# Kernel tuning notes

Hardware: AMD Instinct MI355X
Metric: run time of the kernel (lower is better)

## Reference

```python
import jax, jax.numpy as jnp
import numpy as np

LARGE_NEG = -1000000000.0
D_MODEL = 1024
NUM_HEADS = 16
DEPTH = D_MODEL // NUM_HEADS


def setup_inputs() -> dict:
    key = jax.random.key(0)
    ks = jax.random.split(key, 12)
    B, S, D = 4, 2048, D_MODEL
    scale = 1.0 / np.sqrt(D)
    inp = {
        "v": jax.random.normal(ks[0], (B, S, D), jnp.float32),
        "k": jax.random.normal(ks[1], (B, S, D), jnp.float32),
        "q": jax.random.normal(ks[2], (B, S, D), jnp.float32),
        "mask": jax.random.randint(ks[3], (B, 1, 1, S), 0, 2, jnp.int32),
        "Wq": jax.random.normal(ks[4], (D, D), jnp.float32) * scale,
        "bq": jnp.zeros((D,), jnp.float32),
        "Wk": jax.random.normal(ks[5], (D, D), jnp.float32) * scale,
        "bk": jnp.zeros((D,), jnp.float32),
        "Wv": jax.random.normal(ks[6], (D, D), jnp.float32) * scale,
        "bv": jnp.zeros((D,), jnp.float32),
        "Wo": jax.random.normal(ks[7], (D, D), jnp.float32) * scale,
        "bo": jnp.zeros((D,), jnp.float32),
    }
    return inp


def _split_heads(x):
    # [B, S, D] -> [B, H, S, depth]
    B, S, _ = x.shape
    return x.reshape(B, S, NUM_HEADS, DEPTH).transpose(0, 2, 1, 3)


def reference(v, k, q, mask, Wq, bq, Wk, bk, Wv, bv, Wo, bo):
    B, Sq, D = q.shape
    qh = _split_heads(q @ Wq + bq)  # [B,H,Sq,d]
    kh = _split_heads(k @ Wk + bk)  # [B,H,Sk,d]
    vh = _split_heads(v @ Wv + bv)  # [B,H,Sk,d]
    logits = jnp.einsum('bhqd,bhkd->bhqk', qh, kh) / jnp.sqrt(
        jnp.asarray(DEPTH, jnp.float32))
    logits = logits + mask.astype(jnp.float32) * LARGE_NEG
    attn = jax.nn.softmax(logits, axis=-1)
    ctx = jnp.einsum('bhqk,bhkd->bhqd', attn, vh)
    ctx = ctx.transpose(0, 2, 1, 3).reshape(B, Sq, D)  # concat heads
    return ctx @ Wo + bo
```

## Files before the change

kernel.cpp:

```cpp
#include <hip/hip_runtime.h>


typedef unsigned short ushort_t;
typedef __bf16          b16x8 __attribute__((ext_vector_type(8)));
typedef unsigned short  u16x8 __attribute__((ext_vector_type(8)));
typedef unsigned short  u16x4 __attribute__((ext_vector_type(4)));
typedef unsigned int    u32x4 __attribute__((ext_vector_type(4)));
typedef float           f32x4 __attribute__((ext_vector_type(4)));

#define B_ 4
#define S_ 2048
#define D_ 1024
#define H_ 16
#define DEPTH_ 64
#define LOG2E 1.4426950408889634f

__device__ __forceinline__ unsigned short f2bf(float f) {
  unsigned u = __builtin_bit_cast(unsigned, f);
  u += 0x7FFFu + ((u >> 16) & 1u);
  return (unsigned short)(u >> 16);
}

__device__ __forceinline__ unsigned pack_trunc(float lo, float hi) {
#if __has_builtin(__builtin_amdgcn_perm)
  return __builtin_amdgcn_perm(__builtin_bit_cast(unsigned, hi),
                               __builtin_bit_cast(unsigned, lo), 0x07060302u);
#else
  return (__builtin_bit_cast(unsigned, hi) & 0xFFFF0000u) |
         (__builtin_bit_cast(unsigned, lo) >> 16);
#endif
}

#if __has_builtin(__builtin_amdgcn_exp2f)
#define EXP2F(x) __builtin_amdgcn_exp2f(x)
#else
#define EXP2F(x) exp2f(x)
#endif

#define GLD16(gp, lp) __builtin_amdgcn_global_load_lds( \
    (__attribute__((address_space(1))) void*)(gp),       \
    (__attribute__((address_space(3))) void*)(lp), 16, 0, 0)

#define MFMA_BF16(a, b, c) __builtin_amdgcn_mfma_f32_16x16x32_bf16( \
    __builtin_bit_cast(b16x8, (a)), __builtin_bit_cast(b16x8, (b)), (c), 0, 0, 0)


__global__ void cvt_acts_kernel(const float* __restrict__ q, const float* __restrict__ k,
                                const float* __restrict__ v,
                                ushort_t* __restrict__ qb, ushort_t* __restrict__ kb,
                                ushort_t* __restrict__ vb) {
  const float* src = blockIdx.y == 0 ? q : blockIdx.y == 1 ? k : v;
  ushort_t*    dst = blockIdx.y == 0 ? qb : blockIdx.y == 1 ? kb : vb;
  size_t i = ((size_t)blockIdx.x * 256 + threadIdx.x) * 4;
  float4 f = *(const float4*)(src + i);
  u16x4 o;
  o[0] = f2bf(f.x); o[1] = f2bf(f.y); o[2] = f2bf(f.z); o[3] = f2bf(f.w);
  *(u16x4*)(dst + i) = o;
}

__global__ void cvt_wt_kernel(const float* __restrict__ Wq, const float* __restrict__ Wk,
                              const float* __restrict__ Wv, const float* __restrict__ Wo,
                              ushort_t* __restrict__ Wqt, ushort_t* __restrict__ Wkt,
                              ushort_t* __restrict__ Wvt, ushort_t* __restrict__ Wot) {
  __shared__ float t[32][33];
  const int z = blockIdx.y;
  const float* W = z == 0 ? Wq : z == 1 ? Wk : z == 2 ? Wv : Wo;
  ushort_t*   Wt = z == 0 ? Wqt : z == 1 ? Wkt : z == 2 ? Wvt : Wot;
  const int x = threadIdx.x & 31, y0 = threadIdx.x >> 5;
  const int kt = (blockIdx.x & 31) * 32, nt = (blockIdx.x >> 5) * 32;
#pragma unroll
  for (int r = 0; r < 4; r++) {
    int row = y0 + r * 8;
    t[row][x] = W[(size_t)(kt + row) * D_ + nt + x];
  }
  __syncthreads();
#pragma unroll
  for (int r = 0; r < 4; r++) {
    int row = y0 + r * 8;
    Wt[(size_t)(nt + row) * D_ + kt + x] = f2bf(t[x][row]);
  }
}


__device__ __forceinline__ void gemm_core(const ushort_t* __restrict__ A,
                                          const ushort_t* __restrict__ Bt,
                                          ushort_t* As, ushort_t* Bs,
                                          int tm, int tn, f32x4* acc) {
  const int tid = threadIdx.x;
  const int lane = tid & 63, wid = tid >> 6;
  const int wm = (wid >> 1) * 64, wn = (wid & 1) * 64;
  const int srow = lane >> 2;
  const int scolL = ((lane & 3) ^ ((srow >> 1) & 3)) * 8;
  const int c0 = wid * 2, c1 = c0 + 1;
  const ushort_t* ga0 = A  + (size_t)(tm + c0 * 16 + srow) * D_ + scolL;
  const ushort_t* ga1 = A  + (size_t)(tm + c1 * 16 + srow) * D_ + scolL;
  const ushort_t* gb0 = Bt + (size_t)(tn + c0 * 16 + srow) * D_ + scolL;
  const ushort_t* gb1 = Bt + (size_t)(tn + c1 * 16 + srow) * D_ + scolL;
  ushort_t* lA0 = As + c0 * 512; ushort_t* lA1 = As + c1 * 512;
  ushort_t* lB0 = Bs + c0 * 512; ushort_t* lB1 = Bs + c1 * 512;
  const int fr = lane & 15;
  const int fswz = ((lane >> 4) ^ ((fr >> 1) & 3)) * 8;
#pragma unroll
  for (int i = 0; i < 16; i++) acc[i] = f32x4{0.f, 0.f, 0.f, 0.f};
  for (int k0 = 0; k0 < D_; k0 += 32) {
    __syncthreads();
    GLD16(ga0 + k0, lA0);
    GLD16(ga1 + k0, lA1);
    GLD16(gb0 + k0, lB0);
    GLD16(gb1 + k0, lB1);
    __syncthreads();
    u16x8 af[4], bf[4];
#pragma unroll
    for (int mi = 0; mi < 4; mi++) af[mi] = *(const u16x8*)(As + (wm + mi * 16 + fr) * 32 + fswz);
#pragma unroll
    for (int ni = 0; ni < 4; ni++) bf[ni] = *(const u16x8*)(Bs + (wn + ni * 16 + fr) * 32 + fswz);
#pragma unroll
    for (int mi = 0; mi < 4; mi++)
#pragma unroll
      for (int ni = 0; ni < 4; ni++)
        acc[mi * 4 + ni] = MFMA_BF16(af[mi], bf[ni], acc[mi * 4 + ni]);
  }
}

__device__ __forceinline__ int sigma32(int k5) {
  return ((k5 & 15) >> 2) * 8 + ((k5 >> 4) & 1) * 4 + (k5 & 3);
}

__global__ __launch_bounds__(256, 2) void qkv_gemm_kernel(
    const ushort_t* __restrict__ qb, const ushort_t* __restrict__ kb, const ushort_t* __restrict__ vb,
    const ushort_t* __restrict__ Wqt, const ushort_t* __restrict__ Wkt, const ushort_t* __restrict__ Wvt,
    const float* __restrict__ bq, const float* __restrict__ bk, const float* __restrict__ bv,
    ushort_t* __restrict__ Qh, ushort_t* __restrict__ Kh, ushort_t* __restrict__ Vht) {
  __shared__ __align__(16) ushort_t smem[128 * 136];
  ushort_t* As = smem;
  ushort_t* Bs = smem + 4096;
  const int z = blockIdx.z;
  const ushort_t* A  = z == 0 ? qb : z == 1 ? kb : vb;
  const ushort_t* Bt = z == 0 ? Wqt : z == 1 ? Wkt : Wvt;
  const float* bias  = z == 0 ? bq : z == 1 ? bk : bv;
  const int tn = blockIdx.x * 128, tm = blockIdx.y * 128;
  f32x4 acc[16];
  gemm_core(A, Bt, As, Bs, tm, tn, acc);
  const int lane = threadIdx.x & 63, wid = threadIdx.x >> 6;
  const int wm = (wid >> 1) * 64, wn = (wid & 1) * 64;
  const int fr = lane & 15, rq = (lane >> 4) * 4;
  if (z == 2) {
    __syncthreads();
    ushort_t* trans = smem;
#pragma unroll
    for (int ni = 0; ni < 4; ni++) {
      const int n = wn + ni * 16 + fr;
      const float bb = bias[tn + n];
#pragma unroll
      for (int mi = 0; mi < 4; mi++) {
#pragma unroll
        for (int r = 0; r < 4; r++) {
          const int m = wm + mi * 16 + rq + r;
          const int mp = (m & ~31) + sigma32(m & 31);
          trans[n * 136 + mp] = f2bf(acc[mi * 4 + ni][r] + bb);
        }
      }
    }
    __syncthreads();
    const int n = threadIdx.x >> 1, hf = threadIdx.x & 1;
    const int col = tn + n, hh = col >> 6, dd = col & 63;
    const int bI = tm >> 11, sb = (tm & 2047) + hf * 64;
    ushort_t* dst = Vht + ((size_t)(bI * H_ + hh) * DEPTH_ + dd) * S_ + sb;
    const ushort_t* srcp = trans + n * 136 + hf * 64;
#pragma unroll
    for (int i = 0; i < 8; i++)
      *(u16x8*)(dst + i * 8) = *(const u16x8*)(srcp + i * 8);
  } else {
    ushort_t* outp = (z == 0) ? Qh : Kh;
    const float qscale = (z == 0) ? 0.125f * LOG2E : 1.0f;
#pragma unroll
    for (int ni = 0; ni < 4; ni++) {
      const int col = tn + wn + ni * 16 + fr;
      const float bb = bias[col];
      const int h = col >> 6, dd = col & 63;
#pragma unroll
      for (int mi = 0; mi < 4; mi++) {
#pragma unroll
        for (int r = 0; r < 4; r++) {
          const int m = tm + wm + mi * 16 + rq + r;
          const int b = m >> 11, s = m & 2047;
          outp[((size_t)(b * H_ + h) * S_ + s) * DEPTH_ + dd] =
              f2bf((acc[mi * 4 + ni][r] + bb) * qscale);
        }
      }
    }
  }
}

__global__ __launch_bounds__(256, 2) void out_gemm_kernel(
    const ushort_t* __restrict__ ctx, const ushort_t* __restrict__ Wot,
    const float* __restrict__ bo, float* __restrict__ out) {
  __shared__ __align__(16) ushort_t As[4096], Bs[4096];
  const int tn = blockIdx.x * 128, tm = blockIdx.y * 128;
  f32x4 acc[16];
  gemm_core(ctx, Wot, As, Bs, tm, tn, acc);
  const int lane = threadIdx.x & 63, wid = threadIdx.x >> 6;
  const int wm = (wid >> 1) * 64, wn = (wid & 1) * 64;
  const int fr = lane & 15, rq = (lane >> 4) * 4;
#pragma unroll
  for (int ni = 0; ni < 4; ni++) {
    const int col = tn + wn + ni * 16 + fr;
    const float bb = bo[col];
#pragma unroll
    for (int mi = 0; mi < 4; mi++) {
#pragma unroll
      for (int r = 0; r < 4; r++) {
        const int m = tm + wm + mi * 16 + rq + r;
        out[(size_t)m * D_ + col] = acc[mi * 4 + ni][r] + bb;
      }
    }
  }
}


__global__ __launch_bounds__(256, 4) void attn_kernel(
    const ushort_t* __restrict__ Qh, const ushort_t* __restrict__ Kh,
    const ushort_t* __restrict__ Vht, const int* __restrict__ mask,
    ushort_t* __restrict__ ctx) {
  __shared__ __align__(16) ushort_t Ks[128 * 64];
  __shared__ __align__(16) ushort_t Vs[64 * 128];
  __shared__ __align__(16) float Cm[2048];
  const int tid = threadIdx.x, lane = tid & 63, wid = tid >> 6;
  const int qt = blockIdx.x, bh = blockIdx.y;
  const int b = bh >> 4, h = bh & 15;
  const size_t base = (size_t)bh * (S_ * DEPTH_);
  const int fr = lane & 15, fq = lane >> 4;

  const int* mrow = mask + b * S_;
#pragma unroll
  for (int i = 0; i < 8; i++) {
    const int idx = tid + i * 256;
    Cm[idx] = mrow[idx] ? -1.4427e9f : 0.0f;
  }

  u16x8 qf[2][2];
#pragma unroll
  for (int nq = 0; nq < 2; nq++)
#pragma unroll
    for (int kc = 0; kc < 2; kc++)
      qf[nq][kc] = *(const u16x8*)(Qh + base +
          (size_t)(qt * 128 + wid * 32 + nq * 16 + fr) * DEPTH_ + kc * 32 + fq * 8);

  u16x8 ones_f;
  {
    const unsigned short o = (fr == 0) ? (unsigned short)0x3F80 : (unsigned short)0;
#pragma unroll
    for (int j = 0; j < 8; j++) ones_f[j] = o;
  }

  f32x4 Oa[4][2];
  f32x4 lacc[2];
#pragma unroll
  for (int di = 0; di < 4; di++)
#pragma unroll
    for (int nq = 0; nq < 2; nq++) Oa[di][nq] = f32x4{0.f, 0.f, 0.f, 0.f};
#pragma unroll
  for (int nq = 0; nq < 2; nq++) lacc[nq] = f32x4{0.f, 0.f, 0.f, 0.f};

  const int krow = lane >> 3;
  const int kcolL = ((lane & 7) ^ (krow & 7)) * 8;
  const int vrowc = lane >> 4;
  const int koff0 = ((0 + fq) ^ (fr & 7)) * 8;
  const int koff1 = ((4 + fq) ^ (fr & 7)) * 8;

  for (int kt = 0; kt < 16; kt++) {
    __syncthreads();
#pragma unroll
    for (int c = 0; c < 4; c++) {
      const int ch = wid * 4 + c;
      GLD16(Kh + base + (size_t)(kt * 128 + ch * 8 + krow) * DEPTH_ + kcolL, Ks + ch * 512);
      const int vrow = ch * 4 + vrowc;
      const int vcolL = ((lane & 15) ^ (vrow & 15)) * 8;
      GLD16(Vht + base + (size_t)vrow * S_ + kt * 128 + vcolL, Vs + ch * 512);
    }
    __syncthreads();

#pragma unroll
    for (int ks = 0; ks < 4; ks++) {
      const int nk0 = ks * 2, nk1 = nk0 + 1;
      const ushort_t* kr0 = Ks + (nk0 * 16 + fr) * 64;
      const ushort_t* kr1 = Ks + (nk1 * 16 + fr) * 64;
      const u16x8 a00 = *(const u16x8*)(kr0 + koff0);
      const u16x8 a01 = *(const u16x8*)(kr0 + koff1);
      const u16x8 a10 = *(const u16x8*)(kr1 + koff0);
      const u16x8 a11 = *(const u16x8*)(kr1 + koff1);
      f32x4 st0[2], st1[2];
#pragma unroll
      for (int nq = 0; nq < 2; nq++) {
        f32x4 t = f32x4{0.f, 0.f, 0.f, 0.f};
        t = MFMA_BF16(a00, qf[nq][0], t);
        t = MFMA_BF16(a01, qf[nq][1], t);
        st0[nq] = t;
        f32x4 u = f32x4{0.f, 0.f, 0.f, 0.f};
        u = MFMA_BF16(a10, qf[nq][0], u);
        u = MFMA_BF16(a11, qf[nq][1], u);
        st1[nq] = u;
      }
      const f32x4 cm0 = *(const f32x4*)(Cm + kt * 128 + nk0 * 16 + fq * 4);
      const f32x4 cm1 = *(const f32x4*)(Cm + kt * 128 + nk1 * 16 + fq * 4);
      u16x8 pb[2];
#pragma unroll
      for (int nq = 0; nq < 2; nq++) {
#pragma unroll
        for (int r = 0; r < 4; r++) {
          st0[nq][r] = EXP2F(st0[nq][r] + cm0[r]);
          st1[nq][r] = EXP2F(st1[nq][r] + cm1[r]);
        }
        u32x4 pk;
        pk[0] = pack_trunc(st0[nq][0], st0[nq][1]);
        pk[1] = pack_trunc(st0[nq][2], st0[nq][3]);
        pk[2] = pack_trunc(st1[nq][0], st1[nq][1]);
        pk[3] = pack_trunc(st1[nq][2], st1[nq][3]);
        pb[nq] = __builtin_bit_cast(u16x8, pk);
      }
      const int voff = ((ks * 4 + fq) ^ fr) * 8;
#pragma unroll
      for (int di = 0; di < 4; di++) {
        const u16x8 vf = *(const u16x8*)(Vs + (di * 16 + fr) * 128 + voff);
#pragma unroll
        for (int nq = 0; nq < 2; nq++)
          Oa[di][nq] = MFMA_BF16(vf, pb[nq], Oa[di][nq]);
      }
#pragma unroll
      for (int nq = 0; nq < 2; nq++)
        lacc[nq] = MFMA_BF16(ones_f, pb[nq], lacc[nq]);
    }
  }

#pragma unroll
  for (int nq = 0; nq < 2; nq++) {
    const int lv = __builtin_amdgcn_ds_bpermute(fr * 4, __builtin_bit_cast(int, lacc[nq][0]));
    const float inv = 1.0f / __builtin_bit_cast(float, lv);
    const int sg = qt * 128 + wid * 32 + nq * 16 + fr;
    ushort_t* crow = ctx + ((size_t)(b * S_ + sg)) * D_ + h * DEPTH_;
#pragma unroll
    for (int di = 0; di < 4; di++) {
      u16x4 o4;
#pragma unroll
      for (int r = 0; r < 4; r++) o4[r] = f2bf(Oa[di][nq][r] * inv);
      *(u16x4*)(crow + di * 16 + fq * 4) = o4;
    }
  }
}


extern "C" void kernel_launch(void* const* d_in, const int* in_sizes, int n_in,
                              void* d_out, int out_size, void* d_ws, size_t ws_size,
                              hipStream_t stream) {
  const float* v  = (const float*)d_in[0];
  const float* k  = (const float*)d_in[1];
  const float* q  = (const float*)d_in[2];
  const int* mask = (const int*)d_in[3];
  const float* Wq = (const float*)d_in[4];
  const float* bq = (const float*)d_in[5];
  const float* Wk = (const float*)d_in[6];
  const float* bk = (const float*)d_in[7];
  const float* Wv = (const float*)d_in[8];
  const float* bv = (const float*)d_in[9];
  const float* Wo = (const float*)d_in[10];
  const float* bo = (const float*)d_in[11];
  float* out = (float*)d_out;

  char* ws = (char*)d_ws;
  ushort_t* qb  = (ushort_t*)(ws);
  ushort_t* kb  = (ushort_t*)(ws + (size_t)(16u << 20));
  ushort_t* vb  = (ushort_t*)(ws + (size_t)(32u << 20));
  ushort_t* Wqt = (ushort_t*)(ws + (size_t)(48u << 20));
  ushort_t* Wkt = (ushort_t*)(ws + (size_t)(50u << 20));
  ushort_t* Wvt = (ushort_t*)(ws + (size_t)(52u << 20));
  ushort_t* Wot = (ushort_t*)(ws + (size_t)(54u << 20));
  ushort_t* Qh  = (ushort_t*)(ws + (size_t)(56u << 20));
  ushort_t* Kh  = (ushort_t*)(ws + (size_t)(72u << 20));
  ushort_t* Vht = (ushort_t*)(ws + (size_t)(88u << 20));
  ushort_t* ctx = qb;

  cvt_acts_kernel<<<dim3(8192, 3), 256, 0, stream>>>(q, k, v, qb, kb, vb);
  cvt_wt_kernel<<<dim3(1024, 4), 256, 0, stream>>>(Wq, Wk, Wv, Wo, Wqt, Wkt, Wvt, Wot);
  qkv_gemm_kernel<<<dim3(8, 64, 3), 256, 0, stream>>>(qb, kb, vb, Wqt, Wkt, Wvt,
                                                      bq, bk, bv, Qh, Kh, Vht);
  attn_kernel<<<dim3(16, 64), 256, 0, stream>>>(Qh, Kh, Vht, mask, ctx);
  out_gemm_kernel<<<dim3(8, 64), 256, 0, stream>>>(ctx, Wot, bo, out);
}
```

Measured before the change: 354.3 us.

## Double GEMM K-step to 64 and remap blocks across XCDs for cache locality

The shared GEMM core now loads a 64-wide K slice per iteration with an XOR-swizzled 64-column layout, which halves the number of barrier pairs per tile. The QKV and output GEMMs, and the attention kernel, switch to 1D grids whose block index is remapped so that blocks landing on the same XCD share the same A rows or the same batch-head. This aims to improve L2 reuse on the chiplet layout. The GEMMs also request occupancy 3 and use twice as much LDS per block, which may limit how many blocks actually fit per CU and adds register pressure.

```diff
diff --git a/kernel.cpp b/kernel.cpp
--- a/kernel.cpp
+++ b/kernel.cpp
@@ -89,36 +89,44 @@
   const int tid = threadIdx.x;
   const int lane = tid & 63, wid = tid >> 6;
   const int wm = (wid >> 1) * 64, wn = (wid & 1) * 64;
-  const int srow = lane >> 2;
-  const int scolL = ((lane & 3) ^ ((srow >> 1) & 3)) * 8;
-  const int c0 = wid * 2, c1 = c0 + 1;
-  const ushort_t* ga0 = A  + (size_t)(tm + c0 * 16 + srow) * D_ + scolL;
-  const ushort_t* ga1 = A  + (size_t)(tm + c1 * 16 + srow) * D_ + scolL;
-  const ushort_t* gb0 = Bt + (size_t)(tn + c0 * 16 + srow) * D_ + scolL;
-  const ushort_t* gb1 = Bt + (size_t)(tn + c1 * 16 + srow) * D_ + scolL;
-  ushort_t* lA0 = As + c0 * 512; ushort_t* lA1 = As + c1 * 512;
-  ushort_t* lB0 = Bs + c0 * 512; ushort_t* lB1 = Bs + c1 * 512;
-  const int fr = lane & 15;
-  const int fswz = ((lane >> 4) ^ ((fr >> 1) & 3)) * 8;
+  const int srow = lane >> 3;
+  const int scol = ((lane & 7) ^ srow) * 8;
+  const ushort_t* gA[4];
+  const ushort_t* gB[4];
+#pragma unroll
+  for (int c = 0; c < 4; c++) {
+    const int ch = wid * 4 + c;
+    gA[c] = A  + (size_t)(tm + ch * 8 + srow) * D_ + scol;
+    gB[c] = Bt + (size_t)(tn + ch * 8 + srow) * D_ + scol;
+  }
+  const int fr = lane & 15, fq = lane >> 4;
 #pragma unroll
   for (int i = 0; i < 16; i++) acc[i] = f32x4{0.f, 0.f, 0.f, 0.f};
-  for (int k0 = 0; k0 < D_; k0 += 32) {
-    __syncthreads();
-    GLD16(ga0 + k0, lA0);
-    GLD16(ga1 + k0, lA1);
-    GLD16(gb0 + k0, lB0);
-    GLD16(gb1 + k0, lB1);
-    __syncthreads();
-    u16x8 af[4], bf[4];
-#pragma unroll
-    for (int mi = 0; mi < 4; mi++) af[mi] = *(const u16x8*)(As + (wm + mi * 16 + fr) * 32 + fswz);
-#pragma unroll
-    for (int ni = 0; ni < 4; ni++) bf[ni] = *(const u16x8*)(Bs + (wn + ni * 16 + fr) * 32 + fswz);
-#pragma unroll
-    for (int mi = 0; mi < 4; mi++)
+  for (int k0 = 0; k0 < D_; k0 += 64) {
+    __syncthreads();
+#pragma unroll
+    for (int c = 0; c < 4; c++) {
+      const int ch = wid * 4 + c;
+      GLD16(gA[c] + k0, As + ch * 512);
+      GLD16(gB[c] + k0, Bs + ch * 512);
+    }
+    __syncthreads();
+#pragma unroll
+    for (int kh = 0; kh < 2; kh++) {
+      const int coff = (((kh * 4 + fq) ^ (fr & 7))) * 8;
+      u16x8 af[4], bf[4];
+#pragma unroll
+      for (int mi = 0; mi < 4; mi++)
+        af[mi] = *(const u16x8*)(As + (wm + mi * 16 + fr) * 64 + coff);
 #pragma unroll
       for (int ni = 0; ni < 4; ni++)
-        acc[mi * 4 + ni] = MFMA_BF16(af[mi], bf[ni], acc[mi * 4 + ni]);
+        bf[ni] = *(const u16x8*)(Bs + (wn + ni * 16 + fr) * 64 + coff);
+#pragma unroll
+      for (int mi = 0; mi < 4; mi++)
+#pragma unroll
+        for (int ni = 0; ni < 4; ni++)
+          acc[mi * 4 + ni] = MFMA_BF16(af[mi], bf[ni], acc[mi * 4 + ni]);
+    }
   }
 }
 
@@ -126,19 +134,26 @@
   return ((k5 & 15) >> 2) * 8 + ((k5 >> 4) & 1) * 4 + (k5 & 3);
 }
 
-__global__ __launch_bounds__(256, 2) void qkv_gemm_kernel(
+__device__ __forceinline__ void gemm_tile_swizzle(int bx, int& tm, int& tn) {
+  const int xcd = bx & 7, j = bx >> 3;
+  tn = (j & 7) * 128;
+  tm = (((j >> 3) << 3) | xcd) * 128;
+}
+
+__global__ __launch_bounds__(256, 3) void qkv_gemm_kernel(
     const ushort_t* __restrict__ qb, const ushort_t* __restrict__ kb, const ushort_t* __restrict__ vb,
     const ushort_t* __restrict__ Wqt, const ushort_t* __restrict__ Wkt, const ushort_t* __restrict__ Wvt,
     const float* __restrict__ bq, const float* __restrict__ bk, const float* __restrict__ bv,
     ushort_t* __restrict__ Qh, ushort_t* __restrict__ Kh, ushort_t* __restrict__ Vht) {
   __shared__ __align__(16) ushort_t smem[128 * 136];
   ushort_t* As = smem;
-  ushort_t* Bs = smem + 4096;
+  ushort_t* Bs = smem + 8192;
   const int z = blockIdx.z;
   const ushort_t* A  = z == 0 ? qb : z == 1 ? kb : vb;
   const ushort_t* Bt = z == 0 ? Wqt : z == 1 ? Wkt : Wvt;
   const float* bias  = z == 0 ? bq : z == 1 ? bk : bv;
-  const int tn = blockIdx.x * 128, tm = blockIdx.y * 128;
+  int tm, tn;
+  gemm_tile_swizzle(blockIdx.x, tm, tn);
   f32x4 acc[16];
   gemm_core(A, Bt, As, Bs, tm, tn, acc);
   const int lane = threadIdx.x & 63, wid = threadIdx.x >> 6;
@@ -192,11 +207,12 @@
   }
 }
 
-__global__ __launch_bounds__(256, 2) void out_gemm_kernel(
+__global__ __launch_bounds__(256, 3) void out_gemm_kernel(
     const ushort_t* __restrict__ ctx, const ushort_t* __restrict__ Wot,
     const float* __restrict__ bo, float* __restrict__ out) {
-  __shared__ __align__(16) ushort_t As[4096], Bs[4096];
-  const int tn = blockIdx.x * 128, tm = blockIdx.y * 128;
+  __shared__ __align__(16) ushort_t As[8192], Bs[8192];
+  int tm, tn;
+  gemm_tile_swizzle(blockIdx.x, tm, tn);
   f32x4 acc[16];
   gemm_core(ctx, Wot, As, Bs, tm, tn, acc);
   const int lane = threadIdx.x & 63, wid = threadIdx.x >> 6;
@@ -226,7 +242,10 @@
   __shared__ __align__(16) ushort_t Vs[64 * 128];
   __shared__ __align__(16) float Cm[2048];
   const int tid = threadIdx.x, lane = tid & 63, wid = tid >> 6;
-  const int qt = blockIdx.x, bh = blockIdx.y;
+  const int id = blockIdx.x;
+  const int xcd = id & 7, j = id >> 3;
+  const int qt = j & 15;
+  const int bh = xcd * 8 + (j >> 4);
   const int b = bh >> 4, h = bh & 15;
   const size_t base = (size_t)bh * (S_ * DEPTH_);
   const int fr = lane & 15, fq = lane >> 4;
@@ -250,7 +269,7 @@
   {
     const unsigned short o = (fr == 0) ? (unsigned short)0x3F80 : (unsigned short)0;
 #pragma unroll
-    for (int j = 0; j < 8; j++) ones_f[j] = o;
+    for (int jj = 0; jj < 8; jj++) ones_f[jj] = o;
   }
 
   f32x4 Oa[4][2];
@@ -381,8 +400,8 @@
 
   cvt_acts_kernel<<<dim3(8192, 3), 256, 0, stream>>>(q, k, v, qb, kb, vb);
   cvt_wt_kernel<<<dim3(1024, 4), 256, 0, stream>>>(Wq, Wk, Wv, Wo, Wqt, Wkt, Wvt, Wot);
-  qkv_gemm_kernel<<<dim3(8, 64, 3), 256, 0, stream>>>(qb, kb, vb, Wqt, Wkt, Wvt,
-                                                      bq, bk, bv, Qh, Kh, Vht);
-  attn_kernel<<<dim3(16, 64), 256, 0, stream>>>(Qh, Kh, Vht, mask, ctx);
-  out_gemm_kernel<<<dim3(8, 64), 256, 0, stream>>>(ctx, Wot, bo, out);
-}
+  qkv_gemm_kernel<<<dim3(512, 1, 3), 256, 0, stream>>>(qb, kb, vb, Wqt, Wkt, Wvt,
+                                                       bq, bk, bv, Qh, Kh, Vht);
+  attn_kernel<<<dim3(1024), 256, 0, stream>>>(Qh, Kh, Vht, mask, ctx);
+  out_gemm_kernel<<<dim3(512), 256, 0, stream>>>(ctx, Wot, bo, out);
+}
```

New measurement: 323.7 us. -8.6%, faster.
